# Optimization experiments

Hardware: AMD Instinct MI355X
Metric: run time of the kernel (lower is better)

## Reference

```python
import jax, jax.numpy as jnp
import numpy as np

D_MODEL = 1024
N_HEADS = 16
HEAD_D = D_MODEL // N_HEADS  # d_keys == d_values == 64
B, L = 4, 2048
EPS_CAUSAL = 1e-6


def setup_inputs() -> dict:
    key = jax.random.key(0)
    ks = jax.random.split(key, 11)
    s = 1.0 / np.sqrt(D_MODEL)
    inp = {
        "queries": jax.random.normal(ks[0], (B, L, D_MODEL), jnp.float32),
        "keys": jax.random.normal(ks[1], (B, L, D_MODEL), jnp.float32),
        "values": jax.random.normal(ks[2], (B, L, D_MODEL), jnp.float32),
        # Linear weights stored as [in, out] so y = x @ W + b (same math as torch Linear)
        "Wq": jax.random.uniform(ks[3], (D_MODEL, N_HEADS * HEAD_D), jnp.float32, -s, s),
        "bq": jax.random.uniform(ks[4], (N_HEADS * HEAD_D,), jnp.float32, -s, s),
        "Wk": jax.random.uniform(ks[5], (D_MODEL, N_HEADS * HEAD_D), jnp.float32, -s, s),
        "bk": jax.random.uniform(ks[6], (N_HEADS * HEAD_D,), jnp.float32, -s, s),
        "Wv": jax.random.uniform(ks[7], (D_MODEL, N_HEADS * HEAD_D), jnp.float32, -s, s),
        "bv": jax.random.uniform(ks[8], (N_HEADS * HEAD_D,), jnp.float32, -s, s),
        "Wo": jax.random.uniform(ks[9], (D_MODEL, D_MODEL), jnp.float32, -s, s),
        "bo": jax.random.uniform(ks[10], (D_MODEL,), jnp.float32, -s, s),
    }
    return inp


def _feat(x):
    # feat_proj: elu(x) + 1
    return jax.nn.elu(x) + 1.0


def _causal_linear_attn(qs, ks, vs):
    # qs/ks: [B,L,H,D], vs: [B,L,H,K]; faithful to original (swapped einsum labels,
    # elementwise denominator).
    def step(carry, xs):
        Si, Zi = carry  # Si: [B,H,D,K], Zi: [B,H,D]
        q, k, v = xs    # each [B,H,D]
        Si = Si + jnp.einsum('bhd,bhk->bhdk', k, v)
        Zi = Zi + k
        num = jnp.einsum('bhd,bhkd->bhk', q, Si)      # note label swap, as in source
        Vi = num / (q * Zi + EPS_CAUSAL)               # elementwise denom, as in source
        return (Si, Zi), Vi

    Bn, Ln, H, D = qs.shape
    K = vs.shape[-1]
    Si0 = jnp.zeros((Bn, H, D, K), qs.dtype)
    Zi0 = jnp.zeros((Bn, H, D), qs.dtype)
    xs = (jnp.swapaxes(qs, 0, 1), jnp.swapaxes(ks, 0, 1), jnp.swapaxes(vs, 0, 1))
    _, out = jax.lax.scan(step, (Si0, Zi0), xs)  # out: [L,B,H,K]
    return jnp.swapaxes(out, 0, 1)               # [B,L,H,K]


def reference(queries, keys, values, Wq, bq, Wk, bk, Wv, bv, Wo, bo):
    N, Lq, _ = queries.shape
    H = N_HEADS
    Q = (queries @ Wq + bq).reshape(N, Lq, H, -1)
    Kp = (keys @ Wk + bk).reshape(N, keys.shape[1], H, -1)
    V = (values @ Wv + bv).reshape(N, values.shape[1], H, -1)
    Q_lin = _feat(Q)
    K_lin = _feat(Kp)
    V_lin = _causal_linear_attn(Q_lin, K_lin, V)  # causal=True branch
    new_values = V_lin.reshape(N, Lq, -1)
    return new_values @ Wo + bo
```

## Files before the change

kernel.cpp:

```cpp
#include <hip/hip_runtime.h>
#include <math.h>

#define DM 1024
#define LL 2048
#define BB 4
#define HH 16
#define HD 64
#define CC 64
#define NC (LL / CC)
#define EPSC 1e-6f
#define PS 72

typedef __attribute__((ext_vector_type(8))) short short8;
typedef __attribute__((ext_vector_type(4))) float floatx4;

__device__ __forceinline__ float featf(float x) { return x > 0.f ? x + 1.f : __expf(x); }

__device__ __forceinline__ unsigned short f2bf(float f) {
    unsigned int u = __builtin_bit_cast(unsigned int, f);
    u = (u + 0x7FFFu + ((u >> 16) & 1u)) >> 16;
    return (unsigned short)u;
}
__device__ __forceinline__ float bf2f(unsigned short h) {
    return __builtin_bit_cast(float, (unsigned int)h << 16);
}
__device__ __forceinline__ void split2(float f, unsigned short& h, unsigned short& l) {
    h = f2bf(f);
    l = f2bf(f - bf2f(h));
}

__device__ __forceinline__ void gload_lds16(const void* g, void* l) {
    __builtin_amdgcn_global_load_lds(
        (const __attribute__((address_space(1))) void*)g,
        (__attribute__((address_space(3))) void*)l,
        16, 0, 0);
}

__global__ __launch_bounds__(256) void convert_bf16(
    const float* __restrict__ in, unsigned short* __restrict__ out)
{
    const int i = blockIdx.x * 256 + threadIdx.x;
    const float4 a = ((const float4*)in)[i * 2];
    const float4 b = ((const float4*)in)[i * 2 + 1];
    union { unsigned short s[8]; uint4 v; } o;
    o.s[0] = f2bf(a.x); o.s[1] = f2bf(a.y); o.s[2] = f2bf(a.z); o.s[3] = f2bf(a.w);
    o.s[4] = f2bf(b.x); o.s[5] = f2bf(b.y); o.s[6] = f2bf(b.z); o.s[7] = f2bf(b.w);
    ((uint4*)out)[i] = o.v;
}

__global__ __launch_bounds__(256) void transpose_conv(
    const float* __restrict__ W, unsigned short* __restrict__ Wt)
{
    __shared__ float tile[64][65];
    const int r0 = blockIdx.y * 64, c0 = blockIdx.x * 64;
    const int tid = threadIdx.x;
#pragma unroll
    for (int e = 0; e < 16; ++e) {
        const int idx = e * 256 + tid;
        const int r = idx >> 6, c = idx & 63;
        tile[r][c] = W[(size_t)(r0 + r) * DM + c0 + c];
    }
    __syncthreads();
#pragma unroll
    for (int e = 0; e < 16; ++e) {
        const int idx = e * 256 + tid;
        const int co = idx >> 6, ro = idx & 63;
        Wt[(size_t)(c0 + co) * DM + r0 + ro] = f2bf(tile[ro][co]);
    }
}

__global__ __launch_bounds__(256) void gemm_mfma(
    const unsigned short* __restrict__ X,
    const unsigned short* __restrict__ Wt,
    const float* __restrict__ bias,
    float* __restrict__ Y, int act)
{
    __shared__ __align__(16) unsigned short As[128 * 32];
    __shared__ __align__(16) unsigned short Bs[128 * 32];

    const int tid = threadIdx.x;
    const int lane = tid & 63;
    const int w = tid >> 6;
    const int wr = w >> 1, wc = w & 1;
    const int fm = lane & 15;
    const int fq = lane >> 4;
    const int m0 = blockIdx.y * 128, n0 = blockIdx.x * 128;

    floatx4 acc[4][4];
#pragma unroll
    for (int i = 0; i < 4; ++i)
#pragma unroll
        for (int j = 0; j < 4; ++j) acc[i][j] = (floatx4){0.f, 0.f, 0.f, 0.f};

    const int row0 = tid >> 2;
    const int row1 = row0 + 64;
    const int slot0 = (tid & 3) ^ (row0 & 3);
    const int slot1 = (tid & 3) ^ (row1 & 3);
    const unsigned short* Xa = X + (size_t)(m0 + row0) * DM + slot0 * 8;
    const unsigned short* Xb = X + (size_t)(m0 + row1) * DM + slot1 * 8;
    const unsigned short* Wa = Wt + (size_t)(n0 + row0) * DM + slot0 * 8;
    const unsigned short* Wb = Wt + (size_t)(n0 + row1) * DM + slot1 * 8;

    const int fswz = ((fq ^ (fm & 3)) << 3);

    for (int k0 = 0; k0 < DM; k0 += 32) {
        gload_lds16(Xa + k0, As + (size_t)tid * 8);
        gload_lds16(Xb + k0, As + (size_t)(256 + tid) * 8);
        gload_lds16(Wa + k0, Bs + (size_t)tid * 8);
        gload_lds16(Wb + k0, Bs + (size_t)(256 + tid) * 8);
        __syncthreads();

        short8 af[4], bf[4];
#pragma unroll
        for (int mt = 0; mt < 4; ++mt)
            af[mt] = *(const short8*)(As + (wr * 64 + mt * 16 + fm) * 32 + fswz);
#pragma unroll
        for (int nt = 0; nt < 4; ++nt)
            bf[nt] = *(const short8*)(Bs + (wc * 64 + nt * 16 + fm) * 32 + fswz);
#pragma unroll
        for (int mt = 0; mt < 4; ++mt)
#pragma unroll
            for (int nt = 0; nt < 4; ++nt)
                acc[mt][nt] = __builtin_amdgcn_mfma_f32_16x16x32_bf16(
                    af[mt], bf[nt], acc[mt][nt], 0, 0, 0);
        __syncthreads();
    }

#pragma unroll
    for (int nt = 0; nt < 4; ++nt) {
        const int col = n0 + wc * 64 + nt * 16 + fm;
        const float bv = bias[col];
#pragma unroll
        for (int mt = 0; mt < 4; ++mt) {
            const int rbase = m0 + wr * 64 + mt * 16 + fq * 4;
#pragma unroll
            for (int r = 0; r < 4; ++r) {
                float v = acc[mt][nt][r] + bv;
                if (act) v = featf(v);
                Y[(size_t)(rbase + r) * DM + col] = v;
            }
        }
    }
}

__global__ __launch_bounds__(256) void chunk_state(
    const float* __restrict__ Kf, const float* __restrict__ Vf,
    float* __restrict__ Mstates, float* __restrict__ Zc)
{
    __shared__ __align__(16) char smem[37888];
    unsigned short* KTH = (unsigned short*)(smem);
    unsigned short* KTL = (unsigned short*)(smem + 9216);
    unsigned short* VTH = (unsigned short*)(smem + 18432);
    unsigned short* VTL = (unsigned short*)(smem + 27648);
    float* scratch = (float*)(smem + 36864);

    const int blk = blockIdx.x;
    const int bh = blk / NC, c = blk % NC;
    const int b = bh / HH, h = bh % HH;
    const int tid = threadIdx.x;
    const int w = tid >> 6, lane = tid & 63;
    const int fm = lane & 15, fq = lane >> 4;
    const size_t gbase = ((size_t)(b * LL + c * CC)) * DM + h * HD;

    {
        const int r = tid >> 2, c0 = (tid & 3) * 16;
#pragma unroll
        for (int g = 0; g < 4; ++g) {
            const int cc0 = c0 + g * 4;
            float4 kv = *(const float4*)(Kf + gbase + (size_t)r * DM + cc0);
            float4 vv = *(const float4*)(Vf + gbase + (size_t)r * DM + cc0);
            float ka[4] = {kv.x, kv.y, kv.z, kv.w};
            float va[4] = {vv.x, vv.y, vv.z, vv.w};
#pragma unroll
            for (int e = 0; e < 4; ++e) {
                unsigned short hh, ll;
                split2(ka[e], hh, ll);
                KTH[(cc0 + e) * PS + r] = hh; KTL[(cc0 + e) * PS + r] = ll;
                split2(va[e], hh, ll);
                VTH[(cc0 + e) * PS + r] = hh; VTL[(cc0 + e) * PS + r] = ll;
            }
        }
    }
    {
        const int s = tid >> 6, j = tid & 63;
        float z = 0.f;
#pragma unroll
        for (int t = 0; t < 16; ++t)
            z += Kf[gbase + (size_t)(s * 16 + t) * DM + j];
        scratch[s * 64 + j] = z;
    }
    __syncthreads();

    if (tid < 64) {
        Zc[(size_t)blk * 64 + tid] = scratch[tid] + scratch[64 + tid] +
                                     scratch[128 + tid] + scratch[192 + tid];
    }

    floatx4 acc[4];
#pragma unroll
    for (int nt = 0; nt < 4; ++nt) acc[nt] = (floatx4){0.f, 0.f, 0.f, 0.f};
    short8 aH[2], aL[2];
#pragma unroll
    for (int ks = 0; ks < 2; ++ks) {
        aH[ks] = *(const short8*)(KTH + (16 * w + fm) * PS + ks * 32 + fq * 8);
        aL[ks] = *(const short8*)(KTL + (16 * w + fm) * PS + ks * 32 + fq * 8);
    }
#pragma unroll
    for (int nt = 0; nt < 4; ++nt) {
#pragma unroll
        for (int ks = 0; ks < 2; ++ks) {
            short8 bH = *(const short8*)(VTH + (nt * 16 + fm) * PS + ks * 32 + fq * 8);
            short8 bL = *(const short8*)(VTL + (nt * 16 + fm) * PS + ks * 32 + fq * 8);
            acc[nt] = __builtin_amdgcn_mfma_f32_16x16x32_bf16(aH[ks], bH, acc[nt], 0, 0, 0);
            acc[nt] = __builtin_amdgcn_mfma_f32_16x16x32_bf16(aH[ks], bL, acc[nt], 0, 0, 0);
            acc[nt] = __builtin_amdgcn_mfma_f32_16x16x32_bf16(aL[ks], bH, acc[nt], 0, 0, 0);
        }
    }
    float* Mout = Mstates + (size_t)blk * 4096;
#pragma unroll
    for (int nt = 0; nt < 4; ++nt) {
        const int dv = nt * 16 + fm;
#pragma unroll
        for (int r = 0; r < 4; ++r) {
            const int j = 16 * w + fq * 4 + r;
            Mout[j * 64 + dv] = acc[nt][r];
        }
    }
}

__global__ __launch_bounds__(256) void prefix_state(
    float* __restrict__ Mstates, float* __restrict__ Zc)
{
    const int bh = blockIdx.x >> 4;
    const int slice = blockIdx.x & 15;
    const int off = slice * 256 + threadIdx.x;
    float run = 0.f;
    float* base = Mstates + (size_t)bh * NC * 4096 + off;
    for (int c = 0; c < NC; ++c) {
        const float v = base[(size_t)c * 4096];
        base[(size_t)c * 4096] = run;
        run += v;
    }
    if (slice == 0 && threadIdx.x < 64) {
        float z = 0.f;
        float* zb = Zc + (size_t)bh * NC * 64 + threadIdx.x;
        for (int c = 0; c < NC; ++c) {
            const float v = zb[c * 64];
            zb[c * 64] = z;
            z += v;
        }
    }
}

__global__ __launch_bounds__(256) void chunk_attn(
    const float* __restrict__ Qf, const float* __restrict__ Kf,
    const float* __restrict__ Vf, const float* __restrict__ Mprev,
    const float* __restrict__ Zprev, unsigned short* __restrict__ Outb)
{
    __shared__ __align__(16) char smem[73728];
    unsigned short* QH  = (unsigned short*)(smem);
    unsigned short* QL  = (unsigned short*)(smem + 9216);
    unsigned short* VH  = (unsigned short*)(smem + 18432);
    unsigned short* VL  = (unsigned short*)(smem + 27648);
    unsigned short* KTH = (unsigned short*)(smem + 36864);
    unsigned short* KTL = (unsigned short*)(smem + 46080);
    unsigned short* AH  = (unsigned short*)(smem + 55296);
    unsigned short* AL  = (unsigned short*)(smem + 64512);
    float* Zf      = (float*)(smem + 36864);
    float* scratch = (float*)(smem + 55296);

    const int blk = blockIdx.x;
    const int bh = blk / NC, c = blk % NC;
    const int b = bh / HH, h = bh % HH;
    const int tid = threadIdx.x;
    const int w = tid >> 6, lane = tid & 63;
    const int fm = lane & 15, fq = lane >> 4;
    const size_t gbase = ((size_t)(b * LL + c * CC)) * DM + h * HD;

    const int lr = tid >> 2, lc0 = (tid & 3) * 16;

    float4 mpre[4];
    {
        const float* Mp = Mprev + (size_t)blk * 4096;
#pragma unroll
        for (int g = 0; g < 4; ++g)
            mpre[g] = *(const float4*)(Mp + lr * 64 + lc0 + g * 4);
    }
#pragma unroll
    for (int g = 0; g < 4; ++g) {
        const int cc0 = lc0 + g * 4;
        float4 qv = *(const float4*)(Qf + gbase + (size_t)lr * DM + cc0);
        float4 vv = *(const float4*)(Vf + gbase + (size_t)lr * DM + cc0);
        float4 kv = *(const float4*)(Kf + gbase + (size_t)lr * DM + cc0);
        float qa[4] = {qv.x, qv.y, qv.z, qv.w};
        float va[4] = {vv.x, vv.y, vv.z, vv.w};
        float ka[4] = {kv.x, kv.y, kv.z, kv.w};
        union { unsigned short s[4]; uint2 v; } qh, ql, vh, vl;
#pragma unroll
        for (int e = 0; e < 4; ++e) {
            split2(qa[e], qh.s[e], ql.s[e]);
            split2(va[e], vh.s[e], vl.s[e]);
            unsigned short hh, ll;
            split2(ka[e], hh, ll);
            KTH[(cc0 + e) * PS + lr] = hh;
            KTL[(cc0 + e) * PS + lr] = ll;
        }
        *(uint2*)(QH + lr * PS + cc0) = qh.v;
        *(uint2*)(QL + lr * PS + cc0) = ql.v;
        *(uint2*)(VH + lr * PS + cc0) = vh.v;
        *(uint2*)(VL + lr * PS + cc0) = vl.v;
    }
    const int zs = tid >> 6, zj = tid & 63;
    float zpart[16];
    {
        float run = 0.f;
#pragma unroll
        for (int t = 0; t < 16; ++t) {
            run += Kf[gbase + (size_t)(zs * 16 + t) * DM + zj];
            zpart[t] = run;
        }
        scratch[zs * 64 + zj] = run;
    }
    const float zp = Zprev[(size_t)blk * 64 + zj];
    __syncthreads();

    {
        float off = zp;
        for (int ss = 0; ss < 4; ++ss)
            if (ss < zs) off += scratch[ss * 64 + zj];
#pragma unroll
        for (int t = 0; t < 16; ++t) zpart[t] += off;
    }

    floatx4 acc1[4];
#pragma unroll
    for (int nt = 0; nt < 4; ++nt) acc1[nt] = (floatx4){0.f, 0.f, 0.f, 0.f};
    {
        short8 aH[2], aL[2];
#pragma unroll
        for (int ks = 0; ks < 2; ++ks) {
            aH[ks] = *(const short8*)(QH + (16 * w + fm) * PS + ks * 32 + fq * 8);
            aL[ks] = *(const short8*)(QL + (16 * w + fm) * PS + ks * 32 + fq * 8);
        }
#pragma unroll
        for (int nt = 0; nt < 4; ++nt) {
#pragma unroll
            for (int ks = 0; ks < 2; ++ks) {
                short8 bH = *(const short8*)(VH + (nt * 16 + fm) * PS + ks * 32 + fq * 8);
                short8 bL = *(const short8*)(VL + (nt * 16 + fm) * PS + ks * 32 + fq * 8);
                acc1[nt] = __builtin_amdgcn_mfma_f32_16x16x32_bf16(aH[ks], bH, acc1[nt], 0, 0, 0);
                acc1[nt] = __builtin_amdgcn_mfma_f32_16x16x32_bf16(aH[ks], bL, acc1[nt], 0, 0, 0);
                acc1[nt] = __builtin_amdgcn_mfma_f32_16x16x32_bf16(aL[ks], bH, acc1[nt], 0, 0, 0);
            }
        }
    }
    __syncthreads();

#pragma unroll
    for (int nt = 0; nt < 4; ++nt) {
        const int t = nt * 16 + fm;
#pragma unroll
        for (int r = 0; r < 4; ++r) {
            const int i = 16 * w + fq * 4 + r;
            const float v = (t <= i) ? acc1[nt][r] : 0.f;
            unsigned short hh, ll;
            split2(v, hh, ll);
            AH[i * PS + t] = hh;
            AL[i * PS + t] = ll;
        }
    }
#pragma unroll
    for (int g = 0; g < 4; ++g) {
        const int cc0 = lc0 + g * 4;
        float ma[4] = {mpre[g].x, mpre[g].y, mpre[g].z, mpre[g].w};
        union { unsigned short s[4]; uint2 v; } mh, ml;
#pragma unroll
        for (int e = 0; e < 4; ++e) split2(ma[e], mh.s[e], ml.s[e]);
        *(uint2*)(VH + lr * PS + cc0) = mh.v;
        *(uint2*)(VL + lr * PS + cc0) = ml.v;
    }
    __syncthreads();

    floatx4 acc2[4];
#pragma unroll
    for (int nt = 0; nt < 4; ++nt) acc2[nt] = (floatx4){0.f, 0.f, 0.f, 0.f};
    {
        short8 aH[4], aL[4];
#pragma unroll
        for (int ks = 0; ks < 2; ++ks) {
            aH[ks] = *(const short8*)(QH + (16 * w + fm) * PS + ks * 32 + fq * 8);
            aL[ks] = *(const short8*)(QL + (16 * w + fm) * PS + ks * 32 + fq * 8);
            aH[2 + ks] = *(const short8*)(AH + (16 * w + fm) * PS + ks * 32 + fq * 8);
            aL[2 + ks] = *(const short8*)(AL + (16 * w + fm) * PS + ks * 32 + fq * 8);
        }
#pragma unroll
        for (int nt = 0; nt < 4; ++nt) {
            const int rb = (nt * 16 + fm) * PS + fq * 8;
#pragma unroll
            for (int ks = 0; ks < 4; ++ks) {
                const unsigned short* BH = (ks < 2) ? VH : KTH;
                const unsigned short* BL = (ks < 2) ? VL : KTL;
                const int ko = (ks & 1) * 32;
                short8 bH = *(const short8*)(BH + rb + ko);
                short8 bL = *(const short8*)(BL + rb + ko);
                acc2[nt] = __builtin_amdgcn_mfma_f32_16x16x32_bf16(aH[ks], bH, acc2[nt], 0, 0, 0);
                acc2[nt] = __builtin_amdgcn_mfma_f32_16x16x32_bf16(aH[ks], bL, acc2[nt], 0, 0, 0);
                acc2[nt] = __builtin_amdgcn_mfma_f32_16x16x32_bf16(aL[ks], bH, acc2[nt], 0, 0, 0);
            }
        }
    }
    __syncthreads();

#pragma unroll
    for (int t = 0; t < 16; ++t)
        Zf[(zs * 16 + t) * 64 + zj] = zpart[t];
    __syncthreads();

#pragma unroll
    for (int nt = 0; nt < 4; ++nt) {
        const int j = nt * 16 + fm;
#pragma unroll
        for (int r = 0; r < 4; ++r) {
            const int i = 16 * w + fq * 4 + r;
            const float q = bf2f(QH[i * PS + j]) + bf2f(QL[i * PS + j]);
            const float z = Zf[i * 64 + j];
            const float denom = fmaf(q, z, EPSC);
            Outb[gbase + (size_t)i * DM + j] = f2bf(acc2[nt][r] / denom);
        }
    }
}

extern "C" void kernel_launch(void* const* d_in, const int* in_sizes, int n_in,
                              void* d_out, int out_size, void* d_ws, size_t ws_size,
                              hipStream_t stream)
{
    (void)in_sizes; (void)n_in; (void)out_size; (void)ws_size;

    const float* queries = (const float*)d_in[0];
    const float* keys    = (const float*)d_in[1];
    const float* values  = (const float*)d_in[2];
    const float* Wq = (const float*)d_in[3];
    const float* bq = (const float*)d_in[4];
    const float* Wk = (const float*)d_in[5];
    const float* bk = (const float*)d_in[6];
    const float* Wv = (const float*)d_in[7];
    const float* bv = (const float*)d_in[8];
    const float* Wo = (const float*)d_in[9];
    const float* bo = (const float*)d_in[10];

    char* ws = (char*)d_ws;
    const size_t MB = 1u << 20;
    unsigned short* qb  = (unsigned short*)(ws);
    unsigned short* kb  = (unsigned short*)(ws + 16 * MB);
    unsigned short* vb  = (unsigned short*)(ws + 32 * MB);
    unsigned short* Wqt = (unsigned short*)(ws + 48 * MB);
    unsigned short* Wkt = (unsigned short*)(ws + 50 * MB);
    unsigned short* Wvt = (unsigned short*)(ws + 52 * MB);
    unsigned short* Wot = (unsigned short*)(ws + 54 * MB);
    float* Qf = (float*)(ws + 56 * MB);
    float* Kf = (float*)(ws + 88 * MB);
    float* Vf = (float*)(ws + 120 * MB);
    float* Zc = (float*)(ws + 152 * MB);
    unsigned short* attnb = (unsigned short*)(ws);
    float* Mst = (float*)(ws + 16 * MB);

    const dim3 gblk(256);
    const int NCONV = (BB * LL * DM) / (8 * 256);
    const dim3 gT(16, 16);
    const dim3 gG(DM / 128, (BB * LL) / 128);

    convert_bf16<<<dim3(NCONV), gblk, 0, stream>>>(queries, qb);
    convert_bf16<<<dim3(NCONV), gblk, 0, stream>>>(keys, kb);
    convert_bf16<<<dim3(NCONV), gblk, 0, stream>>>(values, vb);
    transpose_conv<<<gT, gblk, 0, stream>>>(Wq, Wqt);
    transpose_conv<<<gT, gblk, 0, stream>>>(Wk, Wkt);
    transpose_conv<<<gT, gblk, 0, stream>>>(Wv, Wvt);
    transpose_conv<<<gT, gblk, 0, stream>>>(Wo, Wot);

    gemm_mfma<<<gG, gblk, 0, stream>>>(qb, Wqt, bq, Qf, 1);
    gemm_mfma<<<gG, gblk, 0, stream>>>(kb, Wkt, bk, Kf, 1);
    gemm_mfma<<<gG, gblk, 0, stream>>>(vb, Wvt, bv, Vf, 0);

    chunk_state<<<dim3(BB * HH * NC), gblk, 0, stream>>>(Kf, Vf, Mst, Zc);
    prefix_state<<<dim3(BB * HH * 16), gblk, 0, stream>>>(Mst, Zc);
    chunk_attn<<<dim3(BB * HH * NC), gblk, 0, stream>>>(Qf, Kf, Vf, Mst, Zc, attnb);

    gemm_mfma<<<gG, gblk, 0, stream>>>(attnb, Wot, bo, (float*)d_out, 0);
}
```

Before: 369.6 us.

## Write K projection in pre-transposed per-chunk layout and fuse conversion launches

The K projection GEMM now writes its output directly in a per-(batch, head, chunk) transposed tile layout with float4 stores. The chunk kernels can then load K contiguously and write K-transposed into LDS with vector stores instead of scattered transposes. chunk_attn keeps Q fragments in registers, reads the denominator's Q from an fp32 LDS copy, and pads the Z buffer to cut bank conflicts. The three input conversions and the four weight transposes are each merged into a single launch. The trade-off is a more specialised GEMM epilogue and layout coupling between kernels.

```diff
diff --git a/kernel.cpp b/kernel.cpp
--- a/kernel.cpp
+++ b/kernel.cpp
@@ -36,22 +36,34 @@
         16, 0, 0);
 }
 
-__global__ __launch_bounds__(256) void convert_bf16(
-    const float* __restrict__ in, unsigned short* __restrict__ out)
-{
-    const int i = blockIdx.x * 256 + threadIdx.x;
-    const float4 a = ((const float4*)in)[i * 2];
-    const float4 b = ((const float4*)in)[i * 2 + 1];
+__global__ __launch_bounds__(256) void convert3(
+    const float* __restrict__ a, const float* __restrict__ b,
+    const float* __restrict__ c, unsigned short* __restrict__ oa,
+    unsigned short* __restrict__ ob, unsigned short* __restrict__ oc)
+{
+    const int blk = blockIdx.x;
+    const int sel = blk >> 12;
+    const float* src = (sel == 0) ? a : (sel == 1) ? b : c;
+    unsigned short* dst = (sel == 0) ? oa : (sel == 1) ? ob : oc;
+    const int i = (blk & 4095) * 256 + threadIdx.x;
+    const float4 x = ((const float4*)src)[i * 2];
+    const float4 y = ((const float4*)src)[i * 2 + 1];
     union { unsigned short s[8]; uint4 v; } o;
-    o.s[0] = f2bf(a.x); o.s[1] = f2bf(a.y); o.s[2] = f2bf(a.z); o.s[3] = f2bf(a.w);
-    o.s[4] = f2bf(b.x); o.s[5] = f2bf(b.y); o.s[6] = f2bf(b.z); o.s[7] = f2bf(b.w);
-    ((uint4*)out)[i] = o.v;
-}
-
-__global__ __launch_bounds__(256) void transpose_conv(
-    const float* __restrict__ W, unsigned short* __restrict__ Wt)
+    o.s[0] = f2bf(x.x); o.s[1] = f2bf(x.y); o.s[2] = f2bf(x.z); o.s[3] = f2bf(x.w);
+    o.s[4] = f2bf(y.x); o.s[5] = f2bf(y.y); o.s[6] = f2bf(y.z); o.s[7] = f2bf(y.w);
+    ((uint4*)dst)[i] = o.v;
+}
+
+__global__ __launch_bounds__(256) void transpose4(
+    const float* __restrict__ W0, const float* __restrict__ W1,
+    const float* __restrict__ W2, const float* __restrict__ W3,
+    unsigned short* __restrict__ T0, unsigned short* __restrict__ T1,
+    unsigned short* __restrict__ T2, unsigned short* __restrict__ T3)
 {
     __shared__ float tile[64][65];
+    const int sel = blockIdx.z;
+    const float* W = (sel == 0) ? W0 : (sel == 1) ? W1 : (sel == 2) ? W2 : W3;
+    unsigned short* Wt = (sel == 0) ? T0 : (sel == 1) ? T1 : (sel == 2) ? T2 : T3;
     const int r0 = blockIdx.y * 64, c0 = blockIdx.x * 64;
     const int tid = threadIdx.x;
 #pragma unroll
@@ -73,7 +85,7 @@
     const unsigned short* __restrict__ X,
     const unsigned short* __restrict__ Wt,
     const float* __restrict__ bias,
-    float* __restrict__ Y, int act)
+    float* __restrict__ Y, int act, int layout)
 {
     __shared__ __align__(16) unsigned short As[128 * 32];
     __shared__ __align__(16) unsigned short Bs[128 * 32];
@@ -126,25 +138,46 @@
         __syncthreads();
     }
 
-#pragma unroll
-    for (int nt = 0; nt < 4; ++nt) {
-        const int col = n0 + wc * 64 + nt * 16 + fm;
-        const float bv = bias[col];
-#pragma unroll
-        for (int mt = 0; mt < 4; ++mt) {
-            const int rbase = m0 + wr * 64 + mt * 16 + fq * 4;
-#pragma unroll
-            for (int r = 0; r < 4; ++r) {
-                float v = acc[mt][nt][r] + bv;
-                if (act) v = featf(v);
-                Y[(size_t)(rbase + r) * DM + col] = v;
+    if (layout == 0) {
+#pragma unroll
+        for (int nt = 0; nt < 4; ++nt) {
+            const int col = n0 + wc * 64 + nt * 16 + fm;
+            const float bv = bias[col];
+#pragma unroll
+            for (int mt = 0; mt < 4; ++mt) {
+                const int rbase = m0 + wr * 64 + mt * 16 + fq * 4;
+#pragma unroll
+                for (int r = 0; r < 4; ++r) {
+                    float v = acc[mt][nt][r] + bv;
+                    if (act) v = featf(v);
+                    Y[(size_t)(rbase + r) * DM + col] = v;
+                }
             }
         }
+    } else {
+        const int b = m0 >> 11;
+        const int cch = ((m0 & 2047) >> 6) + wr;
+        const int h = (n0 >> 6) + wc;
+        float* base = Y + ((size_t)((b * 16 + h) * 32 + cch)) * 4096;
+#pragma unroll
+        for (int nt = 0; nt < 4; ++nt) {
+            const int j = nt * 16 + fm;
+            const float bv = bias[n0 + wc * 64 + nt * 16 + fm];
+#pragma unroll
+            for (int mt = 0; mt < 4; ++mt) {
+                float4 o;
+                o.x = acc[mt][nt][0] + bv; o.y = acc[mt][nt][1] + bv;
+                o.z = acc[mt][nt][2] + bv; o.w = acc[mt][nt][3] + bv;
+                if (act) { o.x = featf(o.x); o.y = featf(o.y);
+                           o.z = featf(o.z); o.w = featf(o.w); }
+                *(float4*)(base + j * 64 + mt * 16 + fq * 4) = o;
+            }
+        }
     }
 }
 
 __global__ __launch_bounds__(256) void chunk_state(
-    const float* __restrict__ Kf, const float* __restrict__ Vf,
+    const float* __restrict__ Kc, const float* __restrict__ Vf,
     float* __restrict__ Mstates, float* __restrict__ Zc)
 {
     __shared__ __align__(16) char smem[37888];
@@ -158,36 +191,52 @@
     const int bh = blk / NC, c = blk % NC;
     const int b = bh / HH, h = bh % HH;
     const int tid = threadIdx.x;
-    const int w = tid >> 6, lane = tid & 63;
+    const int w = tid >> 6;
+    const int lane = tid & 63;
     const int fm = lane & 15, fq = lane >> 4;
     const size_t gbase = ((size_t)(b * LL + c * CC)) * DM + h * HD;
-
-    {
-        const int r = tid >> 2, c0 = (tid & 3) * 16;
+    const float* Kblk = Kc + (size_t)blk * 4096;
+
+    const int lr = tid >> 2, lc0 = (tid & 3) * 16;
+
+    {
+        float ka[16];
+#pragma unroll
+        for (int g = 0; g < 4; ++g)
+            *(float4*)(ka + g * 4) = *(const float4*)(Kblk + lr * 64 + lc0 + g * 4);
+        union { unsigned short s[16]; uint4 v[2]; } hh, ll;
+#pragma unroll
+        for (int e = 0; e < 16; ++e) split2(ka[e], hh.s[e], ll.s[e]);
+        *(uint4*)(KTH + lr * PS + lc0) = hh.v[0];
+        *(uint4*)(KTH + lr * PS + lc0 + 8) = hh.v[1];
+        *(uint4*)(KTL + lr * PS + lc0) = ll.v[0];
+        *(uint4*)(KTL + lr * PS + lc0 + 8) = ll.v[1];
+    }
+    {
+        float va[16];
+#pragma unroll
+        for (int g = 0; g < 4; ++g)
+            *(float4*)(va + g * 4) = *(const float4*)(Vf + gbase + (size_t)lr * DM + lc0 + g * 4);
+#pragma unroll
+        for (int g = 0; g < 4; ++g)
+#pragma unroll
+            for (int e0 = 0; e0 < 4; ++e0) {
+                const int e = g * 4 + ((e0 + tid) & 3);
+                unsigned short hh, ll;
+                split2(va[e], hh, ll);
+                VTH[(lc0 + e) * PS + lr] = hh;
+                VTL[(lc0 + e) * PS + lr] = ll;
+            }
+    }
+    {
+        const int zj = tid & 63, zs = tid >> 6;
+        float z = 0.f;
 #pragma unroll
         for (int g = 0; g < 4; ++g) {
-            const int cc0 = c0 + g * 4;
-            float4 kv = *(const float4*)(Kf + gbase + (size_t)r * DM + cc0);
-            float4 vv = *(const float4*)(Vf + gbase + (size_t)r * DM + cc0);
-            float ka[4] = {kv.x, kv.y, kv.z, kv.w};
-            float va[4] = {vv.x, vv.y, vv.z, vv.w};
-#pragma unroll
-            for (int e = 0; e < 4; ++e) {
-                unsigned short hh, ll;
-                split2(ka[e], hh, ll);
-                KTH[(cc0 + e) * PS + r] = hh; KTL[(cc0 + e) * PS + r] = ll;
-                split2(va[e], hh, ll);
-                VTH[(cc0 + e) * PS + r] = hh; VTL[(cc0 + e) * PS + r] = ll;
-            }
-        }
-    }
-    {
-        const int s = tid >> 6, j = tid & 63;
-        float z = 0.f;
-#pragma unroll
-        for (int t = 0; t < 16; ++t)
-            z += Kf[gbase + (size_t)(s * 16 + t) * DM + j];
-        scratch[s * 64 + j] = z;
+            float4 kv = *(const float4*)(Kblk + zj * 64 + zs * 16 + g * 4);
+            z += kv.x + kv.y + kv.z + kv.w;
+        }
+        scratch[zs * 64 + zj] = z;
     }
     __syncthreads();
 
@@ -253,21 +302,20 @@
 }
 
 __global__ __launch_bounds__(256) void chunk_attn(
-    const float* __restrict__ Qf, const float* __restrict__ Kf,
+    const float* __restrict__ Qf, const float* __restrict__ Kc,
     const float* __restrict__ Vf, const float* __restrict__ Mprev,
     const float* __restrict__ Zprev, unsigned short* __restrict__ Outb)
 {
-    __shared__ __align__(16) char smem[73728];
-    unsigned short* QH  = (unsigned short*)(smem);
-    unsigned short* QL  = (unsigned short*)(smem + 9216);
-    unsigned short* VH  = (unsigned short*)(smem + 18432);
-    unsigned short* VL  = (unsigned short*)(smem + 27648);
-    unsigned short* KTH = (unsigned short*)(smem + 36864);
-    unsigned short* KTL = (unsigned short*)(smem + 46080);
-    unsigned short* AH  = (unsigned short*)(smem + 55296);
-    unsigned short* AL  = (unsigned short*)(smem + 64512);
-    float* Zf      = (float*)(smem + 36864);
-    float* scratch = (float*)(smem + 55296);
+    __shared__ __align__(16) char smem[72704];
+    unsigned short* VH  = (unsigned short*)(smem);
+    unsigned short* VL  = (unsigned short*)(smem + 9216);
+    unsigned short* KTH = (unsigned short*)(smem + 18432);
+    unsigned short* KTL = (unsigned short*)(smem + 27648);
+    unsigned short* AH  = (unsigned short*)(smem + 36864);
+    unsigned short* AL  = (unsigned short*)(smem + 46080);
+    float* Qs = (float*)(smem + 55296);
+    float* Zf = (float*)(smem + 18432);
+    float* scratch = (float*)(smem + 36864);
 
     const int blk = blockIdx.x;
     const int bh = blk / NC, c = blk % NC;
@@ -276,6 +324,7 @@
     const int w = tid >> 6, lane = tid & 63;
     const int fm = lane & 15, fq = lane >> 4;
     const size_t gbase = ((size_t)(b * LL + c * CC)) * DM + h * HD;
+    const float* Kblk = Kc + (size_t)blk * 4096;
 
     const int lr = tid >> 2, lc0 = (tid & 3) * 16;
 
@@ -286,39 +335,63 @@
         for (int g = 0; g < 4; ++g)
             mpre[g] = *(const float4*)(Mp + lr * 64 + lc0 + g * 4);
     }
-#pragma unroll
-    for (int g = 0; g < 4; ++g) {
-        const int cc0 = lc0 + g * 4;
-        float4 qv = *(const float4*)(Qf + gbase + (size_t)lr * DM + cc0);
-        float4 vv = *(const float4*)(Vf + gbase + (size_t)lr * DM + cc0);
-        float4 kv = *(const float4*)(Kf + gbase + (size_t)lr * DM + cc0);
-        float qa[4] = {qv.x, qv.y, qv.z, qv.w};
-        float va[4] = {vv.x, vv.y, vv.z, vv.w};
-        float ka[4] = {kv.x, kv.y, kv.z, kv.w};
-        union { unsigned short s[4]; uint2 v; } qh, ql, vh, vl;
-#pragma unroll
-        for (int e = 0; e < 4; ++e) {
-            split2(qa[e], qh.s[e], ql.s[e]);
-            split2(va[e], vh.s[e], vl.s[e]);
-            unsigned short hh, ll;
-            split2(ka[e], hh, ll);
-            KTH[(cc0 + e) * PS + lr] = hh;
-            KTL[(cc0 + e) * PS + lr] = ll;
-        }
-        *(uint2*)(QH + lr * PS + cc0) = qh.v;
-        *(uint2*)(QL + lr * PS + cc0) = ql.v;
-        *(uint2*)(VH + lr * PS + cc0) = vh.v;
-        *(uint2*)(VL + lr * PS + cc0) = vl.v;
-    }
-    const int zs = tid >> 6, zj = tid & 63;
+    {
+        float va[16];
+#pragma unroll
+        for (int g = 0; g < 4; ++g)
+            *(float4*)(va + g * 4) = *(const float4*)(Vf + gbase + (size_t)lr * DM + lc0 + g * 4);
+        union { unsigned short s[16]; uint4 v[2]; } hh, ll;
+#pragma unroll
+        for (int e = 0; e < 16; ++e) split2(va[e], hh.s[e], ll.s[e]);
+        *(uint4*)(VH + lr * PS + lc0) = hh.v[0];
+        *(uint4*)(VH + lr * PS + lc0 + 8) = hh.v[1];
+        *(uint4*)(VL + lr * PS + lc0) = ll.v[0];
+        *(uint4*)(VL + lr * PS + lc0 + 8) = ll.v[1];
+    }
+    {
+        float ka[16];
+#pragma unroll
+        for (int g = 0; g < 4; ++g)
+            *(float4*)(ka + g * 4) = *(const float4*)(Kblk + lr * 64 + lc0 + g * 4);
+        union { unsigned short s[16]; uint4 v[2]; } hh, ll;
+#pragma unroll
+        for (int e = 0; e < 16; ++e) split2(ka[e], hh.s[e], ll.s[e]);
+        *(uint4*)(KTH + lr * PS + lc0) = hh.v[0];
+        *(uint4*)(KTH + lr * PS + lc0 + 8) = hh.v[1];
+        *(uint4*)(KTL + lr * PS + lc0) = ll.v[0];
+        *(uint4*)(KTL + lr * PS + lc0 + 8) = ll.v[1];
+    }
+    {
+#pragma unroll
+        for (int g = 0; g < 4; ++g) {
+            float4 qv = *(const float4*)(Qf + gbase + (size_t)lr * DM + lc0 + g * 4);
+            *(float4*)(Qs + lr * 68 + lc0 + g * 4) = qv;
+        }
+    }
+    short8 qH[2], qL[2];
+    {
+        const float* qrow = Qf + gbase + (size_t)(16 * w + fm) * DM;
+#pragma unroll
+        for (int ks = 0; ks < 2; ++ks) {
+            float qa[8];
+            *(float4*)(qa)     = *(const float4*)(qrow + ks * 32 + fq * 8);
+            *(float4*)(qa + 4) = *(const float4*)(qrow + ks * 32 + fq * 8 + 4);
+            union { unsigned short s[8]; short8 v; } hh, ll;
+#pragma unroll
+            for (int e = 0; e < 8; ++e) split2(qa[e], hh.s[e], ll.s[e]);
+            qH[ks] = hh.v; qL[ks] = ll.v;
+        }
+    }
+    const int zj = tid & 63, zs = tid >> 6;
     float zpart[16];
     {
+        float ka[16];
+#pragma unroll
+        for (int g = 0; g < 4; ++g)
+            *(float4*)(ka + g * 4) = *(const float4*)(Kblk + zj * 64 + zs * 16 + g * 4);
         float run = 0.f;
 #pragma unroll
-        for (int t = 0; t < 16; ++t) {
-            run += Kf[gbase + (size_t)(zs * 16 + t) * DM + zj];
-            zpart[t] = run;
-        }
+        for (int t = 0; t < 16; ++t) { run += ka[t]; zpart[t] = run; }
         scratch[zs * 64 + zj] = run;
     }
     const float zp = Zprev[(size_t)blk * 64 + zj];
@@ -335,23 +408,15 @@
     floatx4 acc1[4];
 #pragma unroll
     for (int nt = 0; nt < 4; ++nt) acc1[nt] = (floatx4){0.f, 0.f, 0.f, 0.f};
-    {
-        short8 aH[2], aL[2];
+#pragma unroll
+    for (int nt = 0; nt < 4; ++nt) {
 #pragma unroll
         for (int ks = 0; ks < 2; ++ks) {
-            aH[ks] = *(const short8*)(QH + (16 * w + fm) * PS + ks * 32 + fq * 8);
-            aL[ks] = *(const short8*)(QL + (16 * w + fm) * PS + ks * 32 + fq * 8);
-        }
-#pragma unroll
-        for (int nt = 0; nt < 4; ++nt) {
-#pragma unroll
-            for (int ks = 0; ks < 2; ++ks) {
-                short8 bH = *(const short8*)(VH + (nt * 16 + fm) * PS + ks * 32 + fq * 8);
-                short8 bL = *(const short8*)(VL + (nt * 16 + fm) * PS + ks * 32 + fq * 8);
-                acc1[nt] = __builtin_amdgcn_mfma_f32_16x16x32_bf16(aH[ks], bH, acc1[nt], 0, 0, 0);
-                acc1[nt] = __builtin_amdgcn_mfma_f32_16x16x32_bf16(aH[ks], bL, acc1[nt], 0, 0, 0);
-                acc1[nt] = __builtin_amdgcn_mfma_f32_16x16x32_bf16(aL[ks], bH, acc1[nt], 0, 0, 0);
-            }
+            short8 bH = *(const short8*)(VH + (nt * 16 + fm) * PS + ks * 32 + fq * 8);
+            short8 bL = *(const short8*)(VL + (nt * 16 + fm) * PS + ks * 32 + fq * 8);
+            acc1[nt] = __builtin_amdgcn_mfma_f32_16x16x32_bf16(qH[ks], bH, acc1[nt], 0, 0, 0);
+            acc1[nt] = __builtin_amdgcn_mfma_f32_16x16x32_bf16(qH[ks], bL, acc1[nt], 0, 0, 0);
+            acc1[nt] = __builtin_amdgcn_mfma_f32_16x16x32_bf16(qL[ks], bH, acc1[nt], 0, 0, 0);
         }
     }
     __syncthreads();
@@ -360,7 +425,8 @@
     for (int nt = 0; nt < 4; ++nt) {
         const int t = nt * 16 + fm;
 #pragma unroll
-        for (int r = 0; r < 4; ++r) {
+        for (int r0 = 0; r0 < 4; ++r0) {
+            const int r = (r0 + fm) & 3;
             const int i = 16 * w + fq * 4 + r;
             const float v = (t <= i) ? acc1[nt][r] : 0.f;
             unsigned short hh, ll;
@@ -371,13 +437,12 @@
     }
 #pragma unroll
     for (int g = 0; g < 4; ++g) {
-        const int cc0 = lc0 + g * 4;
         float ma[4] = {mpre[g].x, mpre[g].y, mpre[g].z, mpre[g].w};
         union { unsigned short s[4]; uint2 v; } mh, ml;
 #pragma unroll
         for (int e = 0; e < 4; ++e) split2(ma[e], mh.s[e], ml.s[e]);
-        *(uint2*)(VH + lr * PS + cc0) = mh.v;
-        *(uint2*)(VL + lr * PS + cc0) = ml.v;
+        *(uint2*)(VH + lr * PS + lc0 + g * 4) = mh.v;
+        *(uint2*)(VL + lr * PS + lc0 + g * 4) = ml.v;
     }
     __syncthreads();
 
@@ -385,35 +450,38 @@
 #pragma unroll
     for (int nt = 0; nt < 4; ++nt) acc2[nt] = (floatx4){0.f, 0.f, 0.f, 0.f};
     {
-        short8 aH[4], aL[4];
+        short8 aAH[2], aAL[2];
 #pragma unroll
         for (int ks = 0; ks < 2; ++ks) {
-            aH[ks] = *(const short8*)(QH + (16 * w + fm) * PS + ks * 32 + fq * 8);
-            aL[ks] = *(const short8*)(QL + (16 * w + fm) * PS + ks * 32 + fq * 8);
-            aH[2 + ks] = *(const short8*)(AH + (16 * w + fm) * PS + ks * 32 + fq * 8);
-            aL[2 + ks] = *(const short8*)(AL + (16 * w + fm) * PS + ks * 32 + fq * 8);
+            aAH[ks] = *(const short8*)(AH + (16 * w + fm) * PS + ks * 32 + fq * 8);
+            aAL[ks] = *(const short8*)(AL + (16 * w + fm) * PS + ks * 32 + fq * 8);
         }
 #pragma unroll
         for (int nt = 0; nt < 4; ++nt) {
             const int rb = (nt * 16 + fm) * PS + fq * 8;
 #pragma unroll
-            for (int ks = 0; ks < 4; ++ks) {
-                const unsigned short* BH = (ks < 2) ? VH : KTH;
-                const unsigned short* BL = (ks < 2) ? VL : KTL;
-                const int ko = (ks & 1) * 32;
-                short8 bH = *(const short8*)(BH + rb + ko);
-                short8 bL = *(const short8*)(BL + rb + ko);
-                acc2[nt] = __builtin_amdgcn_mfma_f32_16x16x32_bf16(aH[ks], bH, acc2[nt], 0, 0, 0);
-                acc2[nt] = __builtin_amdgcn_mfma_f32_16x16x32_bf16(aH[ks], bL, acc2[nt], 0, 0, 0);
-                acc2[nt] = __builtin_amdgcn_mfma_f32_16x16x32_bf16(aL[ks], bH, acc2[nt], 0, 0, 0);
+            for (int ks = 0; ks < 2; ++ks) {
+                short8 bH = *(const short8*)(VH + rb + ks * 32);
+                short8 bL = *(const short8*)(VL + rb + ks * 32);
+                acc2[nt] = __builtin_amdgcn_mfma_f32_16x16x32_bf16(qH[ks], bH, acc2[nt], 0, 0, 0);
+                acc2[nt] = __builtin_amdgcn_mfma_f32_16x16x32_bf16(qH[ks], bL, acc2[nt], 0, 0, 0);
+                acc2[nt] = __builtin_amdgcn_mfma_f32_16x16x32_bf16(qL[ks], bH, acc2[nt], 0, 0, 0);
             }
+#pragma unroll
+            for (int ks = 0; ks < 2; ++ks) {
+                short8 bH = *(const short8*)(KTH + rb + ks * 32);
+                short8 bL = *(const short8*)(KTL + rb + ks * 32);
+                acc2[nt] = __builtin_amdgcn_mfma_f32_16x16x32_bf16(aAH[ks], bH, acc2[nt], 0, 0, 0);
+                acc2[nt] = __builtin_amdgcn_mfma_f32_16x16x32_bf16(aAH[ks], bL, acc2[nt], 0, 0, 0);
+                acc2[nt] = __builtin_amdgcn_mfma_f32_16x16x32_bf16(aAL[ks], bH, acc2[nt], 0, 0, 0);
+            }
         }
     }
     __syncthreads();
 
 #pragma unroll
     for (int t = 0; t < 16; ++t)
-        Zf[(zs * 16 + t) * 64 + zj] = zpart[t];
+        Zf[zj * 67 + zs * 16 + t] = zpart[t];
     __syncthreads();
 
 #pragma unroll
@@ -422,8 +490,8 @@
 #pragma unroll
         for (int r = 0; r < 4; ++r) {
             const int i = 16 * w + fq * 4 + r;
-            const float q = bf2f(QH[i * PS + j]) + bf2f(QL[i * PS + j]);
-            const float z = Zf[i * 64 + j];
+            const float q = Qs[i * 68 + j];
+            const float z = Zf[j * 67 + i];
             const float denom = fmaf(q, z, EPSC);
             Outb[gbase + (size_t)i * DM + j] = f2bf(acc2[nt][r] / denom);
         }
@@ -458,32 +526,25 @@
     unsigned short* Wvt = (unsigned short*)(ws + 52 * MB);
     unsigned short* Wot = (unsigned short*)(ws + 54 * MB);
     float* Qf = (float*)(ws + 56 * MB);
-    float* Kf = (float*)(ws + 88 * MB);
+    float* Kc = (float*)(ws + 88 * MB);
     float* Vf = (float*)(ws + 120 * MB);
     float* Zc = (float*)(ws + 152 * MB);
     unsigned short* attnb = (unsigned short*)(ws);
     float* Mst = (float*)(ws + 16 * MB);
 
     const dim3 gblk(256);
-    const int NCONV = (BB * LL * DM) / (8 * 256);
-    const dim3 gT(16, 16);
     const dim3 gG(DM / 128, (BB * LL) / 128);
 
-    convert_bf16<<<dim3(NCONV), gblk, 0, stream>>>(queries, qb);
-    convert_bf16<<<dim3(NCONV), gblk, 0, stream>>>(keys, kb);
-    convert_bf16<<<dim3(NCONV), gblk, 0, stream>>>(values, vb);
-    transpose_conv<<<gT, gblk, 0, stream>>>(Wq, Wqt);
-    transpose_conv<<<gT, gblk, 0, stream>>>(Wk, Wkt);
-    transpose_conv<<<gT, gblk, 0, stream>>>(Wv, Wvt);
-    transpose_conv<<<gT, gblk, 0, stream>>>(Wo, Wot);
-
-    gemm_mfma<<<gG, gblk, 0, stream>>>(qb, Wqt, bq, Qf, 1);
-    gemm_mfma<<<gG, gblk, 0, stream>>>(kb, Wkt, bk, Kf, 1);
-    gemm_mfma<<<gG, gblk, 0, stream>>>(vb, Wvt, bv, Vf, 0);
-
-    chunk_state<<<dim3(BB * HH * NC), gblk, 0, stream>>>(Kf, Vf, Mst, Zc);
+    convert3<<<dim3(3 * 4096), gblk, 0, stream>>>(queries, keys, values, qb, kb, vb);
+    transpose4<<<dim3(16, 16, 4), gblk, 0, stream>>>(Wq, Wk, Wv, Wo, Wqt, Wkt, Wvt, Wot);
+
+    gemm_mfma<<<gG, gblk, 0, stream>>>(qb, Wqt, bq, Qf, 1, 0);
+    gemm_mfma<<<gG, gblk, 0, stream>>>(kb, Wkt, bk, Kc, 1, 1);
+    gemm_mfma<<<gG, gblk, 0, stream>>>(vb, Wvt, bv, Vf, 0, 0);
+
+    chunk_state<<<dim3(BB * HH * NC), gblk, 0, stream>>>(Kc, Vf, Mst, Zc);
     prefix_state<<<dim3(BB * HH * 16), gblk, 0, stream>>>(Mst, Zc);
-    chunk_attn<<<dim3(BB * HH * NC), gblk, 0, stream>>>(Qf, Kf, Vf, Mst, Zc, attnb);
-
-    gemm_mfma<<<gG, gblk, 0, stream>>>(attnb, Wot, bo, (float*)d_out, 0);
-}
+    chunk_attn<<<dim3(BB * HH * NC), gblk, 0, stream>>>(Qf, Kc, Vf, Mst, Zc, attnb);
+
+    gemm_mfma<<<gG, gblk, 0, stream>>>(attnb, Wot, bo, (float*)d_out, 0, 0);
+}
```

New measurement: 369.3 us. About the same (-0.1%).
